# Optimization experiments

Hardware: AMD Instinct MI355X
Metric: run time of the kernel (lower is better)

## Reference

```python
import jax, jax.numpy as jnp
import numpy as np

IN_FEATURES = 4096
OUT_FEATURES = 4096
SHARED_ROWS = 512
BATCH = 4096


def setup_inputs() -> dict:
    key = jax.random.key(0)
    k1, k2, k3 = jax.random.split(key, 3)
    x = jax.random.normal(k1, (BATCH, IN_FEATURES), dtype=jnp.float32)
    shared_weights = jax.random.normal(k2, (SHARED_ROWS, IN_FEATURES), dtype=jnp.float32)
    bias = jax.random.normal(k3, (OUT_FEATURES,), dtype=jnp.float32)
    return {"x": x, "shared_weights": shared_weights, "bias": bias}


def reference(x, shared_weights, bias):
    # Original: W = shared_weights.repeat(out_features // shared_rows, 1)  -> [out, in]
    #           y = x @ W.T + bias
    # Row i of W equals shared_weights[i % shared_rows], so the output columns are a
    # tile of the small GEMM result — compute the small GEMM once and tile (same math,
    # avoids materializing the full [out, in] weight).
    reps = OUT_FEATURES // SHARED_ROWS
    y_small = jnp.einsum("bi,ri->br", x, shared_weights)  # [batch, shared_rows]
    y = jnp.tile(y_small, (1, reps)) + bias  # [batch, out_features]
    return y
```

## Files before the change

### kernel.cpp

```cpp
#include <hip/hip_runtime.h>
#include <hip/hip_bf16.h>


typedef __bf16 bf8 __attribute__((ext_vector_type(8)));
typedef float f4 __attribute__((ext_vector_type(4)));
typedef unsigned int uint;
typedef unsigned short ushort;

constexpr int M = 4096;
constexpr int K = 4096;
constexpr int NS = 512;
constexpr int OUTF = 4096;
constexpr int BM = 64, BN = 64, BK = 64;
constexpr int NITER = K / BK;
constexpr int SSTR = 68;

#define PERM_HI2(hi, lo) __builtin_amdgcn_perm((hi), (lo), 0x07060302u)
#define WAITCNT_VM6 0xF76
#define WAITCNT_VM0 0xF70

__device__ __forceinline__ void async16(const void* g, void* l) {
  __builtin_amdgcn_global_load_lds(
      (const __attribute__((address_space(1))) void*)g,
      (__attribute__((address_space(3))) void*)l, 16, 0, 0);
}

__global__ __launch_bounds__(256)
void convert_w(const float* __restrict__ w, ushort* __restrict__ wb) {
  const size_t i = (size_t)blockIdx.x * 256 + threadIdx.x;
  const float* src = w + i * 8;
  ushort* dst = wb + i * 8;
  const uint4 a = *reinterpret_cast<const uint4*>(src);
  const uint4 b = *reinterpret_cast<const uint4*>(src + 4);
  uint4 o;
  o.x = PERM_HI2(a.y, a.x); o.y = PERM_HI2(a.w, a.z);
  o.z = PERM_HI2(b.y, b.x); o.w = PERM_HI2(b.w, b.z);
  *reinterpret_cast<uint4*>(dst) = o;
}

__global__ __launch_bounds__(256, 2)
void gemm_kernel(const float* __restrict__ x, const ushort* __restrict__ wb,
                 const float* __restrict__ bias, float* __restrict__ out) {
  __shared__ __align__(16) float  As[3][BM * BK];
  __shared__ __align__(16) ushort Bs[3][BN * BK];

  const int b  = blockIdx.x;
  const int mt = ((b >> 6) << 3) | (b & 7);
  const int nt = (b >> 3) & 7;

  const int tid  = threadIdx.x;
  const int wv   = tid >> 6;
  const int lane = tid & 63;

  int goffA[4], llocA[4];
#pragma unroll
  for (int j = 0; j < 4; ++j) {
    const int c = (wv * 4 + j) * 64 + lane;
    const int r = c >> 4;
    const int g = (c & 15) ^ (r & 15);
    goffA[j] = r * K + g * 4;
    llocA[j] = (wv * 4 + j) * 256;
  }
  int goffB[2], llocB[2];
#pragma unroll
  for (int j = 0; j < 2; ++j) {
    const int c = (wv * 2 + j) * 64 + lane;
    const int r = c >> 3;
    const int g = (c & 7) ^ (r & 7);
    goffB[j] = r * K + g * 8;
    llocB[j] = (wv * 2 + j) * 512;
  }

  const float*  xT = x  + (size_t)(mt * BM) * K;
  const ushort* wT = wb + (size_t)(nt * BN) * K;

  const int wm = (wv & 1) * 32;
  const int wn = (wv >> 1) * 32;
  const int lr = lane & 15;
  const int lq = lane >> 4;

  f4 acc[2][2] = {};

  auto issue = [&](int tile, int stage) {
    const int ko = tile * BK;
#pragma unroll
    for (int j = 0; j < 4; ++j)
      async16(xT + ko + goffA[j], &As[stage][llocA[j]]);
#pragma unroll
    for (int j = 0; j < 2; ++j)
      async16(wT + ko + goffB[j], &Bs[stage][llocB[j]]);
  };

  issue(0, 0);
  issue(1, 1);

  int st = 0;
  for (int kk = 0; kk < NITER; ++kk) {
    if (kk + 1 < NITER) __builtin_amdgcn_s_waitcnt(WAITCNT_VM6);
    else                __builtin_amdgcn_s_waitcnt(WAITCNT_VM0);
    __builtin_amdgcn_s_barrier();
    asm volatile("" ::: "memory");

    if (kk + 2 < NITER) {
      int st2 = st + 2; if (st2 >= 3) st2 -= 3;
      issue(kk + 2, st2);
    }

    const float*  aT = As[st];
    const ushort* bT = Bs[st];
#pragma unroll
    for (int t = 0; t < 2; ++t) {
      bf8 af[2], bfv[2];
#pragma unroll
      for (int mf = 0; mf < 2; ++mf) {
        const int row = wm + mf * 16 + lr;
        const int ca  = ((t * 4 + lq) * 2) ^ lr;
        const f4 a0 = *reinterpret_cast<const f4*>(&aT[row * BK + ca * 4]);
        const f4 a1 = *reinterpret_cast<const f4*>(&aT[row * BK + (ca ^ 1) * 4]);
        const uint* u0 = reinterpret_cast<const uint*>(&a0);
        const uint* u1 = reinterpret_cast<const uint*>(&a1);
        uint4 p;
        p.x = PERM_HI2(u0[1], u0[0]); p.y = PERM_HI2(u0[3], u0[2]);
        p.z = PERM_HI2(u1[1], u1[0]); p.w = PERM_HI2(u1[3], u1[2]);
        af[mf] = __builtin_bit_cast(bf8, p);
      }
      const int sc = ((t * 4 + lq) ^ (lr & 7)) * 8;
#pragma unroll
      for (int nf = 0; nf < 2; ++nf)
        bfv[nf] = *reinterpret_cast<const bf8*>(&bT[(wn + nf * 16 + lr) * BK + sc]);
#pragma unroll
      for (int mf = 0; mf < 2; ++mf)
#pragma unroll
        for (int nf = 0; nf < 2; ++nf)
          acc[mf][nf] = __builtin_amdgcn_mfma_f32_16x16x32_bf16(af[mf], bfv[nf], acc[mf][nf], 0, 0, 0);
    }
    asm volatile("" ::: "memory");

    if (++st >= 3) st = 0;
  }

  __syncthreads();
  float* scr = &As[0][0];
#pragma unroll
  for (int mf = 0; mf < 2; ++mf)
#pragma unroll
    for (int nf = 0; nf < 2; ++nf)
#pragma unroll
      for (int r = 0; r < 4; ++r)
        scr[(wm + mf * 16 + lq * 4 + r) * SSTR + wn + nf * 16 + lr] = acc[mf][nf][r];
  __syncthreads();

  const int c4 = tid & 15;
  const int r0 = (tid >> 4) * 4;
  const float4* bias4 = reinterpret_cast<const float4*>(bias);
  float4 bb[8];
#pragma unroll
  for (int rep = 0; rep < 8; ++rep)
    bb[rep] = bias4[rep * 128 + nt * 16 + c4];

#pragma unroll
  for (int rr = 0; rr < 4; ++rr) {
    const int row = r0 + rr;
    const float4 v = *reinterpret_cast<const float4*>(&scr[row * SSTR + c4 * 4]);
    float* orow = out + (size_t)(mt * BM + row) * OUTF + nt * BN + c4 * 4;
#pragma unroll
    for (int rep = 0; rep < 8; ++rep) {
      float4 o;
      o.x = v.x + bb[rep].x; o.y = v.y + bb[rep].y;
      o.z = v.z + bb[rep].z; o.w = v.w + bb[rep].w;
      *reinterpret_cast<float4*>(orow + rep * NS) = o;
    }
  }
}

extern "C" void kernel_launch(void* const* d_in, const int* in_sizes, int n_in,
                              void* d_out, int out_size, void* d_ws, size_t ws_size,
                              hipStream_t stream) {
  (void)in_sizes; (void)n_in; (void)out_size; (void)ws_size;
  const float* x    = (const float*)d_in[0];
  const float* w    = (const float*)d_in[1];
  const float* bias = (const float*)d_in[2];
  float* out = (float*)d_out;

  ushort* wb = (ushort*)d_ws;

  constexpr int convw_blocks = (int)((size_t)NS * K / 8 / 256);
  convert_w<<<dim3(convw_blocks), dim3(256), 0, stream>>>(w, wb);
  gemm_kernel<<<dim3(64 * 8), dim3(256), 0, stream>>>(x, wb, bias, out);
}
```

Baseline: 174.9 us.

## Use 128x128 tiles with 32x32 MFMA and split-K pair exchange via tickets

The GEMM tile grows from 64x64 to 128x128 with 512 threads and switches to the 32x32x16 bf16 MFMA, which raises data reuse per loaded byte. K is split in two so the grid still has 256 blocks. Each split writes its partial sums into a different output replica region, then the pair synchronises through per-tile atomic tickets that convert_w resets. Each block then adds its partner's partial plus bias and writes half of the 8 tiled replicas. The spin-wait assumes both halves of a pair are co-resident, which can deadlock if they are not, and the output round-trip adds memory traffic.

```diff
diff --git a/kernel.cpp b/kernel.cpp
--- a/kernel.cpp
+++ b/kernel.cpp
@@ -4,6 +4,7 @@
 
 typedef __bf16 bf8 __attribute__((ext_vector_type(8)));
 typedef float f4 __attribute__((ext_vector_type(4)));
+typedef float f16v __attribute__((ext_vector_type(16)));
 typedef unsigned int uint;
 typedef unsigned short ushort;
 
@@ -11,12 +12,16 @@
 constexpr int K = 4096;
 constexpr int NS = 512;
 constexpr int OUTF = 4096;
-constexpr int BM = 64, BN = 64, BK = 64;
-constexpr int NITER = K / BK;
-constexpr int SSTR = 68;
+constexpr int BM = 128, BN = 128, BK = 32;
+constexpr int SPLITS = 2;
+constexpr int KSPL = K / SPLITS;
+constexpr int NITER = KSPL / BK;
+constexpr int MT = M / BM;
+constexpr int NT = NS / BN;
+constexpr int NTILES = MT * NT;
 
 #define PERM_HI2(hi, lo) __builtin_amdgcn_perm((hi), (lo), 0x07060302u)
-#define WAITCNT_VM6 0xF76
+#define WAITCNT_VM3 0xF73
 #define WAITCNT_VM0 0xF70
 
 __device__ __forceinline__ void async16(const void* g, void* l) {
@@ -26,7 +31,9 @@
 }
 
 __global__ __launch_bounds__(256)
-void convert_w(const float* __restrict__ w, ushort* __restrict__ wb) {
+void convert_w(const float* __restrict__ w, ushort* __restrict__ wb,
+               uint* __restrict__ tickets) {
+  if (blockIdx.x == 0 && threadIdx.x < NTILES) tickets[threadIdx.x] = 0u;
   const size_t i = (size_t)blockIdx.x * 256 + threadIdx.x;
   const float* src = w + i * 8;
   ushort* dst = wb + i * 8;
@@ -38,139 +45,138 @@
   *reinterpret_cast<uint4*>(dst) = o;
 }
 
-__global__ __launch_bounds__(256, 2)
+__global__ __launch_bounds__(512, 1)
 void gemm_kernel(const float* __restrict__ x, const ushort* __restrict__ wb,
-                 const float* __restrict__ bias, float* __restrict__ out) {
+                 const float* __restrict__ bias, float* __restrict__ out,
+                 uint* __restrict__ tickets) {
   __shared__ __align__(16) float  As[3][BM * BK];
   __shared__ __align__(16) ushort Bs[3][BN * BK];
 
-  const int b  = blockIdx.x;
-  const int mt = ((b >> 6) << 3) | (b & 7);
-  const int nt = (b >> 3) & 7;
+  const int b   = blockIdx.x;
+  const int low = b & 7, h = b >> 3;
+  const int mt  = (h >> 3) * 8 + low;
+  const int nt  = h & 3;
+  const int sp  = (h >> 2) & 1;
 
   const int tid  = threadIdx.x;
   const int wv   = tid >> 6;
   const int lane = tid & 63;
+  const int l31  = lane & 31;
+  const int hi   = lane >> 5;
 
-  int goffA[4], llocA[4];
-#pragma unroll
-  for (int j = 0; j < 4; ++j) {
-    const int c = (wv * 4 + j) * 64 + lane;
-    const int r = c >> 4;
-    const int g = (c & 15) ^ (r & 15);
-    goffA[j] = r * K + g * 4;
-    llocA[j] = (wv * 4 + j) * 256;
-  }
-  int goffB[2], llocB[2];
+  int goffA[2], llocA[2];
 #pragma unroll
   for (int j = 0; j < 2; ++j) {
     const int c = (wv * 2 + j) * 64 + lane;
-    const int r = c >> 3;
-    const int g = (c & 7) ^ (r & 7);
-    goffB[j] = r * K + g * 8;
-    llocB[j] = (wv * 2 + j) * 512;
+    const int r = c >> 3, g = (c & 7) ^ (r & 7);
+    goffA[j] = r * K + g * 4;
+    llocA[j] = c * 4;
+  }
+  int goffB, llocB;
+  {
+    const int c = wv * 64 + lane;
+    const int r = c >> 2, g = (c & 3) ^ ((r >> 1) & 3);
+    goffB = r * K + g * 8;
+    llocB = c * 8;
   }
 
-  const float*  xT = x  + (size_t)(mt * BM) * K;
-  const ushort* wT = wb + (size_t)(nt * BN) * K;
+  const float*  xT = x  + (size_t)(mt * BM) * K + sp * KSPL;
+  const ushort* wT = wb + (size_t)(nt * BN) * K + sp * KSPL;
 
-  const int wm = (wv & 1) * 32;
-  const int wn = (wv >> 1) * 32;
-  const int lr = lane & 15;
-  const int lq = lane >> 4;
-
-  f4 acc[2][2] = {};
-
-  auto issue = [&](int tile, int stage) {
+  auto issue = [&](int tile, int stg) {
     const int ko = tile * BK;
 #pragma unroll
-    for (int j = 0; j < 4; ++j)
-      async16(xT + ko + goffA[j], &As[stage][llocA[j]]);
-#pragma unroll
-    for (int j = 0; j < 2; ++j)
-      async16(wT + ko + goffB[j], &Bs[stage][llocB[j]]);
+    for (int j = 0; j < 2; ++j) async16(xT + ko + goffA[j], &As[stg][llocA[j]]);
+    async16(wT + ko + goffB, &Bs[stg][llocB]);
   };
+
+  const int wm   = (wv & 3) * 32;
+  const int wn   = (wv >> 2) * 64;
+  const int rowA = wm + l31;
+  const int axor = l31 & 7;
+  const int bxor = (l31 >> 1) & 3;
+  const int rb0  = wn + l31, rb1 = wn + 32 + l31;
+
+  f16v acc[2] = {};
 
   issue(0, 0);
   issue(1, 1);
 
   int st = 0;
   for (int kk = 0; kk < NITER; ++kk) {
-    if (kk + 1 < NITER) __builtin_amdgcn_s_waitcnt(WAITCNT_VM6);
+    if (kk + 1 < NITER) __builtin_amdgcn_s_waitcnt(WAITCNT_VM3);
     else                __builtin_amdgcn_s_waitcnt(WAITCNT_VM0);
     __builtin_amdgcn_s_barrier();
     asm volatile("" ::: "memory");
-
     if (kk + 2 < NITER) {
-      int st2 = st + 2; if (st2 >= 3) st2 -= 3;
-      issue(kk + 2, st2);
+      int s2 = st + 2; if (s2 >= 3) s2 -= 3;
+      issue(kk + 2, s2);
     }
 
     const float*  aT = As[st];
     const ushort* bT = Bs[st];
 #pragma unroll
-    for (int t = 0; t < 2; ++t) {
-      bf8 af[2], bfv[2];
-#pragma unroll
-      for (int mf = 0; mf < 2; ++mf) {
-        const int row = wm + mf * 16 + lr;
-        const int ca  = ((t * 4 + lq) * 2) ^ lr;
-        const f4 a0 = *reinterpret_cast<const f4*>(&aT[row * BK + ca * 4]);
-        const f4 a1 = *reinterpret_cast<const f4*>(&aT[row * BK + (ca ^ 1) * 4]);
-        const uint* u0 = reinterpret_cast<const uint*>(&a0);
-        const uint* u1 = reinterpret_cast<const uint*>(&a1);
-        uint4 p;
-        p.x = PERM_HI2(u0[1], u0[0]); p.y = PERM_HI2(u0[3], u0[2]);
-        p.z = PERM_HI2(u1[1], u1[0]); p.w = PERM_HI2(u1[3], u1[2]);
-        af[mf] = __builtin_bit_cast(bf8, p);
-      }
-      const int sc = ((t * 4 + lq) ^ (lr & 7)) * 8;
-#pragma unroll
-      for (int nf = 0; nf < 2; ++nf)
-        bfv[nf] = *reinterpret_cast<const bf8*>(&bT[(wn + nf * 16 + lr) * BK + sc]);
-#pragma unroll
-      for (int mf = 0; mf < 2; ++mf)
-#pragma unroll
-        for (int nf = 0; nf < 2; ++nf)
-          acc[mf][nf] = __builtin_amdgcn_mfma_f32_16x16x32_bf16(af[mf], bfv[nf], acc[mf][nf], 0, 0, 0);
+    for (int ks = 0; ks < 2; ++ks) {
+      const int q0 = (ks * 2 + hi) * 2;
+      const int ca = q0 ^ axor;
+      const f4 a0 = *reinterpret_cast<const f4*>(&aT[rowA * BK + ca * 4]);
+      const f4 a1 = *reinterpret_cast<const f4*>(&aT[rowA * BK + (ca ^ 1) * 4]);
+      const uint* u0 = reinterpret_cast<const uint*>(&a0);
+      const uint* u1 = reinterpret_cast<const uint*>(&a1);
+      uint4 p;
+      p.x = PERM_HI2(u0[1], u0[0]); p.y = PERM_HI2(u0[3], u0[2]);
+      p.z = PERM_HI2(u1[1], u1[0]); p.w = PERM_HI2(u1[3], u1[2]);
+      const bf8 af = __builtin_bit_cast(bf8, p);
+      const int cb = ks * 2 + hi;
+      const bf8 b0 = *reinterpret_cast<const bf8*>(&bT[rb0 * BK + (cb ^ bxor) * 8]);
+      const bf8 b1 = *reinterpret_cast<const bf8*>(&bT[rb1 * BK + (cb ^ bxor) * 8]);
+      acc[0] = __builtin_amdgcn_mfma_f32_32x32x16_bf16(af, b0, acc[0], 0, 0, 0);
+      acc[1] = __builtin_amdgcn_mfma_f32_32x32x16_bf16(af, b1, acc[1], 0, 0, 0);
     }
     asm volatile("" ::: "memory");
-
     if (++st >= 3) st = 0;
   }
 
+  const int colb = nt * BN + wn;
+  float* obase = out + (size_t)(mt * BM + wm) * OUTF;
+
+#pragma unroll
+  for (int n = 0; n < 2; ++n)
+#pragma unroll
+    for (int j = 0; j < 16; ++j) {
+      const int rowf = (j & 3) + 8 * (j >> 2) + 4 * hi;
+      obase[(size_t)rowf * OUTF + sp * NS + colb + n * 32 + l31] = acc[n][j];
+    }
+
   __syncthreads();
-  float* scr = &As[0][0];
-#pragma unroll
-  for (int mf = 0; mf < 2; ++mf)
-#pragma unroll
-    for (int nf = 0; nf < 2; ++nf)
-#pragma unroll
-      for (int r = 0; r < 4; ++r)
-        scr[(wm + mf * 16 + lq * 4 + r) * SSTR + wn + nf * 16 + lr] = acc[mf][nf][r];
+  if (tid == 0) {
+    uint* tk = &tickets[mt * NT + nt];
+    __hip_atomic_fetch_add(tk, 1u, __ATOMIC_ACQ_REL, __HIP_MEMORY_SCOPE_AGENT);
+    while (__hip_atomic_load(tk, __ATOMIC_ACQUIRE, __HIP_MEMORY_SCOPE_AGENT) < SPLITS)
+      __builtin_amdgcn_s_sleep(2);
+  }
   __syncthreads();
 
-  const int c4 = tid & 15;
-  const int r0 = (tid >> 4) * 4;
-  const float4* bias4 = reinterpret_cast<const float4*>(bias);
-  float4 bb[8];
+  const int po = (sp ^ 1) * NS;
+  float bv[2][4];
 #pragma unroll
-  for (int rep = 0; rep < 8; ++rep)
-    bb[rep] = bias4[rep * 128 + nt * 16 + c4];
+  for (int n = 0; n < 2; ++n)
+#pragma unroll
+    for (int i = 0; i < 4; ++i)
+      bv[n][i] = bias[(2 * i + (sp ^ 1)) * NS + colb + n * 32 + l31];
 
 #pragma unroll
-  for (int rr = 0; rr < 4; ++rr) {
-    const int row = r0 + rr;
-    const float4 v = *reinterpret_cast<const float4*>(&scr[row * SSTR + c4 * 4]);
-    float* orow = out + (size_t)(mt * BM + row) * OUTF + nt * BN + c4 * 4;
+  for (int n = 0; n < 2; ++n)
 #pragma unroll
-    for (int rep = 0; rep < 8; ++rep) {
-      float4 o;
-      o.x = v.x + bb[rep].x; o.y = v.y + bb[rep].y;
-      o.z = v.z + bb[rep].z; o.w = v.w + bb[rep].w;
-      *reinterpret_cast<float4*>(orow + rep * NS) = o;
+    for (int j = 0; j < 16; ++j) {
+      const int rowf = (j & 3) + 8 * (j >> 2) + 4 * hi;
+      const float s =
+          acc[n][j] + obase[(size_t)rowf * OUTF + po + colb + n * 32 + l31];
+#pragma unroll
+      for (int i = 0; i < 4; ++i)
+        obase[(size_t)rowf * OUTF + (2 * i + (sp ^ 1)) * NS + colb + n * 32 + l31] =
+            s + bv[n][i];
     }
-  }
 }
 
 extern "C" void kernel_launch(void* const* d_in, const int* in_sizes, int n_in,
@@ -183,8 +189,9 @@
   float* out = (float*)d_out;
 
   ushort* wb = (ushort*)d_ws;
+  uint* tickets = (uint*)(wb + (size_t)NS * K);
 
   constexpr int convw_blocks = (int)((size_t)NS * K / 8 / 256);
-  convert_w<<<dim3(convw_blocks), dim3(256), 0, stream>>>(w, wb);
-  gemm_kernel<<<dim3(64 * 8), dim3(256), 0, stream>>>(x, wb, bias, out);
+  convert_w<<<dim3(convw_blocks), dim3(256), 0, stream>>>(w, wb, tickets);
+  gemm_kernel<<<dim3(NTILES * SPLITS), dim3(512), 0, stream>>>(x, wb, bias, out, tickets);
 }
```

Result: slower. 212.6 us (+21.6%).
